# Kernel optimization log

Hardware: AMD Instinct MI355X
Metric: run time of the kernel (lower is better)

## Reference

```python
import jax, jax.numpy as jnp
import numpy as np

NUM_GROUPS = 64  # matches fill_max of ids; all groups present w.h.p. so unique-inverse == ids


def setup_inputs() -> dict:
    key = jax.random.key(0)
    ks = jax.random.split(key, 8)
    B, N, D = 8, 8192, 512
    s = 1.0 / np.sqrt(D)
    return {
        "x": jax.random.normal(ks[0], (B, N, D), dtype=jnp.float32),
        "ids": jax.random.randint(ks[1], (N,), 0, NUM_GROUPS),
        "w1": jax.random.normal(ks[2], (D, D), dtype=jnp.float32) * s,
        "b1": jax.random.normal(ks[3], (D,), dtype=jnp.float32) * s,
        "w2": jax.random.normal(ks[4], (D, D), dtype=jnp.float32) * s,
        "b2": jax.random.normal(ks[5], (D,), dtype=jnp.float32) * s,
        "w3": jax.random.normal(ks[6], (D, D), dtype=jnp.float32) * s,
        "b3": jax.random.normal(ks[7], (D,), dtype=jnp.float32) * s,
    }


def reference(x, ids, w1, b1, w2, b2, w3, b3):
    # x: [B, N, D]; ids: [N] group labels in [0, NUM_GROUPS)
    G = NUM_GROUPS
    a = jnp.einsum('bnd,ed->bne', x, w1) + b1          # linear1 logits
    v = jnp.einsum('bnd,ed->bne', x, w2) + b2          # linear2 values
    # move segment axis to front: [N, B, D]
    aT = jnp.transpose(a, (1, 0, 2))
    vT = jnp.transpose(v, (1, 0, 2))
    # per-group stable softmax along the segment axis
    mx = jax.lax.stop_gradient(jax.ops.segment_max(aT, ids, num_segments=G))  # [G,B,D]
    ex = jnp.exp(aT - mx[ids])
    denom = jax.ops.segment_sum(ex, ids, num_segments=G)                      # [G,B,D]
    wts = ex / denom[ids]                                                     # [N,B,D]
    # weighted scatter-sum of values -> [G, B, D] -> [B, G, D]
    y = jnp.transpose(jax.ops.segment_sum(vT * wts, ids, num_segments=G), (1, 0, 2))
    out = jnp.einsum('bgd,ed->bge', y, w3) + b3        # linear3
    # expand: gather group outputs back to per-element rows -> [B, N, D]
    return out[:, ids]
```

## Files before the change

### kernel.cpp

```cpp
#include <hip/hip_runtime.h>
#include <hip/hip_bf16.h>
#include <math.h>

#define B_ 8
#define N_ 8192
#define D_ 512
#define G_ 64
#define M_ (B_ * N_)

typedef short bf16x8 __attribute__((ext_vector_type(8)));
typedef float f32x4 __attribute__((ext_vector_type(4)));

__device__ __forceinline__ unsigned short f2bf(float f) {
    __hip_bfloat16 h = __float2bfloat16(f);
    return *reinterpret_cast<unsigned short*>(&h);
}
__device__ __forceinline__ void gload_lds16(const void* g, void* l) {
    __builtin_amdgcn_global_load_lds((const __attribute__((address_space(1))) void*)g,
                                     (__attribute__((address_space(3))) void*)l,
                                     16, 0, 0);
}

__global__ __launch_bounds__(256) void bl_all(const int* __restrict__ ids,
                                              int* __restrict__ counts,
                                              int* __restrict__ baseO,
                                              int* __restrict__ fgO,
                                              int* __restrict__ perm) {
    __shared__ int sid[N_];
    __shared__ unsigned short hist[256][G_];
    __shared__ int sb[G_ + 1];
    __shared__ int cnts[G_];
    const int g = blockIdx.x;
    const int t = threadIdx.x;
    for (int i = t; i < N_; i += 256) sid[i] = ids[i];
#pragma unroll
    for (int gg = 0; gg < G_; ++gg) hist[t][gg] = 0;
    __syncthreads();
    const int nb = t * 32;
    for (int k = 0; k < 32; ++k) hist[t][sid[nb + k]]++;
    __syncthreads();
    if (t < G_) {
        int run = 0;
        for (int i = 0; i < 256; ++i) {
            int v = hist[i][t];
            hist[i][t] = (unsigned short)run;
            run += v;
        }
        cnts[t] = run;
    }
    __syncthreads();
    if (t == 0) {
        int a = 0;
        for (int gg = 0; gg < G_; ++gg) { sb[gg] = a; a += cnts[gg]; }
        sb[G_] = a;
    }
    __syncthreads();
    if (g == 0 && t < G_) {
        counts[t] = cnts[t];
        baseO[t] = sb[t];
        const int row = t * 128;
        int gg = 0;
        while (gg + 1 < G_ && sb[gg + 1] <= row) ++gg;
        fgO[t] = gg;
    }
    int pos = sb[g] + hist[t][g];
    for (int k = 0; k < 32; ++k)
        if (sid[nb + k] == g) perm[pos++] = nb + k;
}

__global__ __launch_bounds__(256) void cast_all(const float* __restrict__ x,
                                                const int* __restrict__ perm,
                                                const float* __restrict__ w1,
                                                const float* __restrict__ b1,
                                                const float* __restrict__ w2,
                                                const float* __restrict__ b2,
                                                unsigned short* __restrict__ xb,
                                                unsigned short* __restrict__ wB,
                                                float* __restrict__ biasB) {
    const int bid = blockIdx.x;
    if (bid < 512) {
        int t = bid * 256 + threadIdx.x;
        int idx = t * 4;
        int row = idx >> 9;
        int col = idx & 511;
        const float* src = (row < 512) ? (w1 + (size_t)row * 512 + col)
                                       : (w2 + (size_t)(row - 512) * 512 + col);
        float4 f = *(const float4*)src;
        ushort4 u;
        u.x = f2bf(f.x); u.y = f2bf(f.y); u.z = f2bf(f.z); u.w = f2bf(f.w);
        *(ushort4*)(wB + idx) = u;
        if (t < 1024) biasB[t] = (t < 512) ? b1[t] : b2[t - 512];
    } else {
        const int total = M_ * 128;
        for (int idx = (bid - 512) * 256 + threadIdx.x; idx < total;
             idx += 2048 * 256) {
            const int row = idx >> 7;
            const int q = (idx & 127) * 4;
            const int b = row >> 13;
            const int i = row & 8191;
            const float* src = x + (((size_t)(b << 13) + perm[i]) << 9) + q;
            float4 f = *(const float4*)src;
            ushort4 u;
            u.x = f2bf(f.x); u.y = f2bf(f.y); u.z = f2bf(f.z); u.w = f2bf(f.w);
            *(ushort4*)(xb + ((size_t)row << 9) + q) = u;
        }
    }
}

__global__ __launch_bounds__(512, 2) void gemm_fused(const unsigned short* __restrict__ xb,
                                                     const unsigned short* __restrict__ wB,
                                                     const float* __restrict__ biasB,
                                                     const int* __restrict__ base,
                                                     const int* __restrict__ fg,
                                                     float* __restrict__ pt) {
    extern __shared__ unsigned short smem[];
    unsigned short* lsA = smem;
    unsigned short* lsB = smem + 32768;

    const int o  = blockIdx.x;
    const int mt = (o & 7) + ((o >> 5) << 3);
    const int nt = (o >> 3) & 3;
    const int b  = mt >> 5;
    const int tlb = (mt & 31) * 2;
    const int c0 = nt * 128;

    const int tid = threadIdx.x;
    const int l = tid & 63;
    const int w = tid >> 6;
    const int wm = w >> 2;
    const int wn = w & 3;
    const int lr = l >> 3;
    const int lslot = l & 7;
    const int fr = l & 15;
    const int kq = l >> 4;
    const int scol = 8 * (lslot ^ lr);

    f32x4 acc[8][4];
#pragma unroll
    for (int i = 0; i < 8; ++i)
#pragma unroll
        for (int j = 0; j < 4; ++j) acc[i][j] = (f32x4){0.f, 0.f, 0.f, 0.f};

    const size_t abase = (((size_t)b << 13) + (size_t)(mt & 31) * 256) << 9;

    auto stageT = [&](int buf, int kt) {
#pragma unroll
        for (int q = 0; q < 4; ++q) {
            const int c = w * 4 + q;
            const int row = c * 8 + lr;
            gload_lds16(xb + abase + ((size_t)row << 9) + kt + scol,
                        lsA + buf * 16384 + c * 512);
        }
#pragma unroll
        for (int q = 0; q < 4; ++q) {
            const int c = w * 4 + q;
            const int srcrow = ((c >> 2) & 1) * 512 + c0 + (c >> 3) * 32
                             + (c & 3) * 8 + lr;
            gload_lds16(wB + ((size_t)srcrow << 9) + kt + scol,
                        lsB + buf * 16384 + c * 512);
        }
    };

    stageT(0, 0);
    __syncthreads();
    int cur = 0;
    for (int t8 = 0; t8 < 8; ++t8) {
        if (t8 < 7) stageT(cur ^ 1, (t8 + 1) * 64);
        const unsigned short* pA = lsA + cur * 16384;
        const unsigned short* pB = lsB + cur * 16384;
        const int ib0 = 8 * (kq ^ (fr & 7));
        const int ib1 = 8 * ((4 + kq) ^ (fr & 7));
        bf16x8 bq0[4], bq1[4];
#pragma unroll
        for (int j = 0; j < 4; ++j) {
            const int brow = (wn * 64 + j * 16 + fr) * 64;
            bq0[j] = *(const bf16x8*)&pB[brow + ib0];
            bq1[j] = *(const bf16x8*)&pB[brow + ib1];
        }
#pragma unroll
        for (int i = 0; i < 8; ++i) {
            const int arow = (wm * 128 + i * 16 + fr) * 64;
            bf16x8 a0 = *(const bf16x8*)&pA[arow + ib0];
            bf16x8 a1 = *(const bf16x8*)&pA[arow + ib1];
#pragma unroll
            for (int j = 0; j < 4; ++j)
                acc[i][j] = __builtin_amdgcn_mfma_f32_16x16x32_bf16(a0, bq0[j], acc[i][j], 0, 0, 0);
#pragma unroll
            for (int j = 0; j < 4; ++j)
                acc[i][j] = __builtin_amdgcn_mfma_f32_16x16x32_bf16(a1, bq1[j], acc[i][j], 0, 0, 0);
        }
        __syncthreads();
        cur ^= 1;
    }

    const int tl = tlb + wm;
    const int fg0 = fg[tl];
    const int bnd0 = (fg0 + 1 < G_) ? base[fg0 + 1] : (1 << 30);
    const int bnd1 = (fg0 + 2 < G_) ? base[fg0 + 2] : (1 << 30);
    const int bnd2 = (fg0 + 3 < G_) ? base[fg0 + 3] : (1 << 30);
    float b1c[2], b2c[2];
#pragma unroll
    for (int j = 0; j < 2; ++j) {
        const int col = c0 + wn * 32 + j * 16 + fr;
        b1c[j] = biasB[col];
        b2c[j] = biasB[512 + col];
    }
    float dp[4][2] = {}, yp[4][2] = {};
    const int rbase = tl * 128 + kq * 4;
#pragma unroll
    for (int i = 0; i < 8; ++i)
#pragma unroll
        for (int rr = 0; rr < 4; ++rr) {
            const int row = rbase + i * 16 + rr;
            const int s = (row >= bnd0) + (row >= bnd1) + (row >= bnd2);
#pragma unroll
            for (int j = 0; j < 2; ++j) {
                const float e = __expf(acc[i][j][rr] + b1c[j]);
                const float ey = e * (acc[i][j + 2][rr] + b2c[j]);
#pragma unroll
                for (int s2 = 0; s2 < 4; ++s2) {
                    dp[s2][j] += (s == s2) ? e : 0.f;
                    yp[s2][j] += (s == s2) ? ey : 0.f;
                }
            }
        }
#pragma unroll
    for (int s2 = 0; s2 < 4; ++s2)
#pragma unroll
        for (int j = 0; j < 2; ++j) {
            dp[s2][j] += __shfl_xor(dp[s2][j], 16);
            dp[s2][j] += __shfl_xor(dp[s2][j], 32);
            yp[s2][j] += __shfl_xor(yp[s2][j], 16);
            yp[s2][j] += __shfl_xor(yp[s2][j], 32);
        }
    if (kq == 0) {
#pragma unroll
        for (int s2 = 0; s2 < 4; ++s2)
#pragma unroll
            for (int j = 0; j < 2; ++j) {
                const int colp = c0 + wn * 32 + j * 16 + fr;
                float2 v = make_float2(dp[s2][j], yp[s2][j]);
                *(float2*)&pt[(((size_t)(b * 64 + tl) * 4 + s2) * 512 + colp) * 2] = v;
            }
    }
}

__global__ __launch_bounds__(256) void combineC(const float* __restrict__ pt,
                                                const int* __restrict__ base,
                                                const int* __restrict__ counts,
                                                const int* __restrict__ fg,
                                                float* __restrict__ y) {
    const int g = blockIdx.x, b = blockIdx.y;
    const int bs = base[g];
    int cnt = counts[g];
    if (cnt == 0) cnt = 1;
    const int t0 = bs >> 7, t1 = (bs + cnt - 1) >> 7;
    for (int c = threadIdx.x; c < 512; c += 256) {
        float d = 0.f, yy = 0.f;
        for (int t = t0; t <= t1; ++t) {
            const int s = g - fg[t];
            if (s >= 0 && s < 4) {
                const float* p = &pt[((((size_t)(b * 64 + t)) * 4 + s) * 512 + c) * 2];
                d += p[0];
                yy += p[1];
            }
        }
        y[((size_t)(b * G_ + g)) * 512 + c] = yy / d;
    }
}

__global__ __launch_bounds__(256) void gemm3(const float* __restrict__ y,
                                             const float* __restrict__ w3,
                                             const float* __restrict__ b3,
                                             float* __restrict__ out_small) {
    __shared__ float ys[16][68];
    __shared__ float wss[16][68];
    const int m0 = blockIdx.x * 64;
    const int n0 = blockIdx.y * 64;
    const int tid = threadIdx.x;
    const int tr = tid >> 4;
    const int tc = tid & 15;
    const int lrow = tid >> 2;
    const int lk4 = (tid & 3) * 4;

    float acc[4][4] = {};

    for (int k0 = 0; k0 < D_; k0 += 16) {
        float4 yv = *(const float4*)(y + (size_t)(m0 + lrow) * D_ + k0 + lk4);
        float4 wv = *(const float4*)(w3 + (size_t)(n0 + lrow) * D_ + k0 + lk4);
        __syncthreads();
        ys[lk4 + 0][lrow] = yv.x;  ys[lk4 + 1][lrow] = yv.y;
        ys[lk4 + 2][lrow] = yv.z;  ys[lk4 + 3][lrow] = yv.w;
        wss[lk4 + 0][lrow] = wv.x; wss[lk4 + 1][lrow] = wv.y;
        wss[lk4 + 2][lrow] = wv.z; wss[lk4 + 3][lrow] = wv.w;
        __syncthreads();
#pragma unroll
        for (int kk = 0; kk < 16; ++kk) {
            float4 y4 = *(const float4*)&ys[kk][tr * 4];
            float4 w4 = *(const float4*)&wss[kk][tc * 4];
            float ya[4] = {y4.x, y4.y, y4.z, y4.w};
            float wa[4] = {w4.x, w4.y, w4.z, w4.w};
#pragma unroll
            for (int i = 0; i < 4; ++i)
#pragma unroll
                for (int j = 0; j < 4; ++j)
                    acc[i][j] = fmaf(ya[i], wa[j], acc[i][j]);
        }
    }

    float bb[4];
#pragma unroll
    for (int j = 0; j < 4; ++j) bb[j] = b3[n0 + tc * 4 + j];
#pragma unroll
    for (int i = 0; i < 4; ++i) {
        size_t o = (size_t)(m0 + tr * 4 + i) * D_ + n0 + tc * 4;
        float4 r;
        r.x = acc[i][0] + bb[0]; r.y = acc[i][1] + bb[1];
        r.z = acc[i][2] + bb[2]; r.w = acc[i][3] + bb[3];
        *(float4*)(out_small + o) = r;
    }
}

__global__ __launch_bounds__(256) void gather_out(const int* __restrict__ ids,
                                                  const float* __restrict__ out_small,
                                                  float* __restrict__ out) {
    const int c = blockIdx.x * 256 + threadIdx.x;
    const int per_row = D_ / 4;
    const int b = c / (N_ * per_row);
    const int rem = c % (N_ * per_row);
    const int n = rem / per_row;
    const int q = rem % per_row;
    const int g = ids[n];
    float4 val = *(const float4*)(out_small + ((size_t)b * G_ + g) * D_ + q * 4);
    *(float4*)(out + (size_t)c * 4) = val;
}

extern "C" void kernel_launch(void* const* d_in, const int* in_sizes, int n_in,
                              void* d_out, int out_size, void* d_ws, size_t ws_size,
                              hipStream_t stream) {
    (void)in_sizes; (void)n_in; (void)out_size; (void)ws_size;
    const float* x   = (const float*)d_in[0];
    const int*   ids = (const int*)d_in[1];
    const float* w1  = (const float*)d_in[2];
    const float* b1  = (const float*)d_in[3];
    const float* w2  = (const float*)d_in[4];
    const float* b2  = (const float*)d_in[5];
    const float* w3  = (const float*)d_in[6];
    const float* b3  = (const float*)d_in[7];
    float* out = (float*)d_out;

    float* ws_f = (float*)d_ws;
    unsigned short* xb = (unsigned short*)ws_f;
    float* after_xb  = ws_f + 16777216;
    unsigned short* wB = (unsigned short*)after_xb;
    float* biasB     = after_xb + 262144;
    float* pt        = biasB + 1024;
    float* y         = pt + 2097152;
    float* out_small = y + 262144;
    int*   perm      = (int*)(out_small + 262144);
    int*   base      = perm + N_;
    int*   counts    = base + G_;
    int*   fg        = counts + G_;

    hipFuncSetAttribute((const void*)gemm_fused,
                        hipFuncAttributeMaxDynamicSharedMemorySize, 131072);

    hipLaunchKernelGGL(bl_all, dim3(G_), dim3(256), 0, stream, ids, counts, base, fg, perm);
    hipLaunchKernelGGL(cast_all, dim3(2560), dim3(256), 0, stream,
                       x, perm, w1, b1, w2, b2, xb, wB, biasB);
    hipLaunchKernelGGL(gemm_fused, dim3(1024), dim3(512), 131072, stream,
                       xb, wB, biasB, base, fg, pt);
    hipLaunchKernelGGL(combineC, dim3(G_, B_), dim3(256), 0, stream, pt, base, counts, fg, y);
    hipLaunchKernelGGL(gemm3, dim3(8, 8), dim3(256), 0, stream, y, w3, b3, out_small);
    hipLaunchKernelGGL(gather_out, dim3(32768), dim3(256), 0, stream, ids, out_small, out);
}
```

Before: 193.3 us.

## Triple-buffer GEMM LDS pipeline with narrower N tiles and explicit vmcnt waits

The fused GEMM+softmax-reduction kernel moves from double to triple buffering. Each iteration issues loads two tiles ahead and waits with explicit s_waitcnt vmcnt counts plus raw barriers. The per-block N tile is halved (64 columns each of logits and values) and the grid doubled, which cuts accumulator registers. LDS use grows to 144KB and occupancy drops to one block per CU, trading occupancy for deeper prefetch and more blocks, each of which re-reads the A tile.

```diff
diff --git a/kernel.cpp b/kernel.cpp
--- a/kernel.cpp
+++ b/kernel.cpp
@@ -20,6 +20,7 @@
                                      (__attribute__((address_space(3))) void*)l,
                                      16, 0, 0);
 }
+#define SBAR() do { __builtin_amdgcn_s_barrier(); __builtin_amdgcn_sched_barrier(0); } while (0)
 
 __global__ __launch_bounds__(256) void bl_all(const int* __restrict__ ids,
                                               int* __restrict__ counts,
@@ -107,7 +108,7 @@
     }
 }
 
-__global__ __launch_bounds__(512, 2) void gemm_fused(const unsigned short* __restrict__ xb,
+__global__ __launch_bounds__(512, 1) void gemm_fused(const unsigned short* __restrict__ xb,
                                                      const unsigned short* __restrict__ wB,
                                                      const float* __restrict__ biasB,
                                                      const int* __restrict__ base,
@@ -115,14 +116,14 @@
                                                      float* __restrict__ pt) {
     extern __shared__ unsigned short smem[];
     unsigned short* lsA = smem;
-    unsigned short* lsB = smem + 32768;
+    unsigned short* lsB = smem + 3 * 16384;
 
     const int o  = blockIdx.x;
-    const int mt = (o & 7) + ((o >> 5) << 3);
-    const int nt = (o >> 3) & 3;
+    const int mt = (o & 7) + ((o >> 6) << 3);
+    const int nt = (o >> 3) & 7;
     const int b  = mt >> 5;
     const int tlb = (mt & 31) * 2;
-    const int c0 = nt * 128;
+    const int c0 = nt * 64;
 
     const int tid = threadIdx.x;
     const int l = tid & 63;
@@ -135,11 +136,12 @@
     const int kq = l >> 4;
     const int scol = 8 * (lslot ^ lr);
 
-    f32x4 acc[8][4];
-#pragma unroll
-    for (int i = 0; i < 8; ++i)
-#pragma unroll
-        for (int j = 0; j < 4; ++j) acc[i][j] = (f32x4){0.f, 0.f, 0.f, 0.f};
+    f32x4 acc[8][2];
+#pragma unroll
+    for (int i = 0; i < 8; ++i) {
+        acc[i][0] = (f32x4){0.f, 0.f, 0.f, 0.f};
+        acc[i][1] = (f32x4){0.f, 0.f, 0.f, 0.f};
+    }
 
     const size_t abase = (((size_t)b << 13) + (size_t)(mt & 31) * 256) << 9;
 
@@ -152,45 +154,41 @@
                         lsA + buf * 16384 + c * 512);
         }
 #pragma unroll
-        for (int q = 0; q < 4; ++q) {
-            const int c = w * 4 + q;
-            const int srcrow = ((c >> 2) & 1) * 512 + c0 + (c >> 3) * 32
-                             + (c & 3) * 8 + lr;
+        for (int q = 0; q < 2; ++q) {
+            const int c = w * 2 + q;
+            const int br = c * 8 + lr;
+            const int srcrow = (c >> 3) * 512 + c0 + (br & 63);
             gload_lds16(wB + ((size_t)srcrow << 9) + kt + scol,
-                        lsB + buf * 16384 + c * 512);
+                        lsB + buf * 8192 + c * 512);
         }
     };
 
     stageT(0, 0);
-    __syncthreads();
-    int cur = 0;
+    stageT(1, 64);
+
+#pragma unroll
     for (int t8 = 0; t8 < 8; ++t8) {
-        if (t8 < 7) stageT(cur ^ 1, (t8 + 1) * 64);
-        const unsigned short* pA = lsA + cur * 16384;
-        const unsigned short* pB = lsB + cur * 16384;
-        const int ib0 = 8 * (kq ^ (fr & 7));
-        const int ib1 = 8 * ((4 + kq) ^ (fr & 7));
-        bf16x8 bq0[4], bq1[4];
-#pragma unroll
-        for (int j = 0; j < 4; ++j) {
-            const int brow = (wn * 64 + j * 16 + fr) * 64;
-            bq0[j] = *(const bf16x8*)&pB[brow + ib0];
-            bq1[j] = *(const bf16x8*)&pB[brow + ib1];
-        }
-#pragma unroll
-        for (int i = 0; i < 8; ++i) {
-            const int arow = (wm * 128 + i * 16 + fr) * 64;
-            bf16x8 a0 = *(const bf16x8*)&pA[arow + ib0];
-            bf16x8 a1 = *(const bf16x8*)&pA[arow + ib1];
-#pragma unroll
-            for (int j = 0; j < 4; ++j)
-                acc[i][j] = __builtin_amdgcn_mfma_f32_16x16x32_bf16(a0, bq0[j], acc[i][j], 0, 0, 0);
-#pragma unroll
-            for (int j = 0; j < 4; ++j)
-                acc[i][j] = __builtin_amdgcn_mfma_f32_16x16x32_bf16(a1, bq1[j], acc[i][j], 0, 0, 0);
-        }
-        __syncthreads();
-        cur ^= 1;
+        SBAR();
+        if (t8 < 6) stageT((t8 + 2) % 3, (t8 + 2) * 64);
+        if (t8 < 6)      asm volatile("s_waitcnt vmcnt(12)" ::: "memory");
+        else if (t8 == 6) asm volatile("s_waitcnt vmcnt(6)" ::: "memory");
+        else              asm volatile("s_waitcnt vmcnt(0)" ::: "memory");
+        __builtin_amdgcn_sched_barrier(0);
+        SBAR();
+        const unsigned short* pA = lsA + (t8 % 3) * 16384;
+        const unsigned short* pB = lsB + (t8 % 3) * 8192;
+#pragma unroll
+        for (int ks = 0; ks < 2; ++ks) {
+            const int ib = 8 * ((ks * 4 + kq) ^ (fr & 7));
+            bf16x8 ba = *(const bf16x8*)&pB[(wn * 16 + fr) * 64 + ib];
+            bf16x8 bv = *(const bf16x8*)&pB[(64 + wn * 16 + fr) * 64 + ib];
+#pragma unroll
+            for (int i = 0; i < 8; ++i) {
+                bf16x8 a = *(const bf16x8*)&pA[(wm * 128 + i * 16 + fr) * 64 + ib];
+                acc[i][0] = __builtin_amdgcn_mfma_f32_16x16x32_bf16(a, ba, acc[i][0], 0, 0, 0);
+                acc[i][1] = __builtin_amdgcn_mfma_f32_16x16x32_bf16(a, bv, acc[i][1], 0, 0, 0);
+            }
+        }
     }
 
     const int tl = tlb + wm;
@@ -198,14 +196,10 @@
     const int bnd0 = (fg0 + 1 < G_) ? base[fg0 + 1] : (1 << 30);
     const int bnd1 = (fg0 + 2 < G_) ? base[fg0 + 2] : (1 << 30);
     const int bnd2 = (fg0 + 3 < G_) ? base[fg0 + 3] : (1 << 30);
-    float b1c[2], b2c[2];
-#pragma unroll
-    for (int j = 0; j < 2; ++j) {
-        const int col = c0 + wn * 32 + j * 16 + fr;
-        b1c[j] = biasB[col];
-        b2c[j] = biasB[512 + col];
-    }
-    float dp[4][2] = {}, yp[4][2] = {};
+    const int colp = c0 + wn * 16 + fr;
+    const float b1c = biasB[colp];
+    const float b2c = biasB[512 + colp];
+    float dp[4] = {}, yp[4] = {};
     const int rbase = tl * 128 + kq * 4;
 #pragma unroll
     for (int i = 0; i < 8; ++i)
@@ -213,35 +207,27 @@
         for (int rr = 0; rr < 4; ++rr) {
             const int row = rbase + i * 16 + rr;
             const int s = (row >= bnd0) + (row >= bnd1) + (row >= bnd2);
-#pragma unroll
-            for (int j = 0; j < 2; ++j) {
-                const float e = __expf(acc[i][j][rr] + b1c[j]);
-                const float ey = e * (acc[i][j + 2][rr] + b2c[j]);
-#pragma unroll
-                for (int s2 = 0; s2 < 4; ++s2) {
-                    dp[s2][j] += (s == s2) ? e : 0.f;
-                    yp[s2][j] += (s == s2) ? ey : 0.f;
-                }
+            const float e = __expf(acc[i][0][rr] + b1c);
+            const float ey = e * (acc[i][1][rr] + b2c);
+#pragma unroll
+            for (int s2 = 0; s2 < 4; ++s2) {
+                dp[s2] += (s == s2) ? e : 0.f;
+                yp[s2] += (s == s2) ? ey : 0.f;
             }
         }
 #pragma unroll
-    for (int s2 = 0; s2 < 4; ++s2)
-#pragma unroll
-        for (int j = 0; j < 2; ++j) {
-            dp[s2][j] += __shfl_xor(dp[s2][j], 16);
-            dp[s2][j] += __shfl_xor(dp[s2][j], 32);
-            yp[s2][j] += __shfl_xor(yp[s2][j], 16);
-            yp[s2][j] += __shfl_xor(yp[s2][j], 32);
-        }
+    for (int s2 = 0; s2 < 4; ++s2) {
+        dp[s2] += __shfl_xor(dp[s2], 16);
+        dp[s2] += __shfl_xor(dp[s2], 32);
+        yp[s2] += __shfl_xor(yp[s2], 16);
+        yp[s2] += __shfl_xor(yp[s2], 32);
+    }
     if (kq == 0) {
 #pragma unroll
-        for (int s2 = 0; s2 < 4; ++s2)
-#pragma unroll
-            for (int j = 0; j < 2; ++j) {
-                const int colp = c0 + wn * 32 + j * 16 + fr;
-                float2 v = make_float2(dp[s2][j], yp[s2][j]);
-                *(float2*)&pt[(((size_t)(b * 64 + tl) * 4 + s2) * 512 + colp) * 2] = v;
-            }
+        for (int s2 = 0; s2 < 4; ++s2) {
+            float2 v = make_float2(dp[s2], yp[s2]);
+            *(float2*)&pt[(((size_t)(b * 64 + tl) * 4 + s2) * 512 + colp) * 2] = v;
+        }
     }
 }
 
@@ -363,12 +349,12 @@
     int*   fg        = counts + G_;
 
     hipFuncSetAttribute((const void*)gemm_fused,
-                        hipFuncAttributeMaxDynamicSharedMemorySize, 131072);
+                        hipFuncAttributeMaxDynamicSharedMemorySize, 147456);
 
     hipLaunchKernelGGL(bl_all, dim3(G_), dim3(256), 0, stream, ids, counts, base, fg, perm);
     hipLaunchKernelGGL(cast_all, dim3(2560), dim3(256), 0, stream,
                        x, perm, w1, b1, w2, b2, xb, wB, biasB);
-    hipLaunchKernelGGL(gemm_fused, dim3(1024), dim3(512), 131072, stream,
+    hipLaunchKernelGGL(gemm_fused, dim3(2048), dim3(512), 147456, stream,
                        xb, wB, biasB, base, fg, pt);
     hipLaunchKernelGGL(combineC, dim3(G_, B_), dim3(256), 0, stream, pt, base, counts, fg, y);
     hipLaunchKernelGGL(gemm3, dim3(8, 8), dim3(256), 0, stream, y, w3, b3, out_small);
```

Result: slower. 207.2 us (+7.2%).

## Load weight fragments directly into registers, halving LDS use in fused GEMM

Applied to the files above, without the earlier changes.

The weight (B) tile is no longer staged through shared memory. Each lane now loads its MFMA B fragments straight from global memory into double-buffered registers, prefetching the next k-step. This halves dynamic LDS from 128KB to 64KB, which may allow more blocks per CU and removes the LDS reads for B. The cost is uncoalesced-ish global loads, duplicated B loads across the waves that share a column slice, and extra register pressure under launch_bounds(512,2).

```diff
diff --git a/kernel.cpp b/kernel.cpp
--- a/kernel.cpp
+++ b/kernel.cpp
@@ -115,7 +115,6 @@
                                                      float* __restrict__ pt) {
     extern __shared__ unsigned short smem[];
     unsigned short* lsA = smem;
-    unsigned short* lsB = smem + 32768;
 
     const int o  = blockIdx.x;
     const int mt = (o & 7) + ((o >> 5) << 3);
@@ -151,32 +150,37 @@
             gload_lds16(xb + abase + ((size_t)row << 9) + kt + scol,
                         lsA + buf * 16384 + c * 512);
         }
-#pragma unroll
-        for (int q = 0; q < 4; ++q) {
-            const int c = w * 4 + q;
-            const int srcrow = ((c >> 2) & 1) * 512 + c0 + (c >> 3) * 32
-                             + (c & 3) * 8 + lr;
-            gload_lds16(wB + ((size_t)srcrow << 9) + kt + scol,
-                        lsB + buf * 16384 + c * 512);
-        }
     };
 
+    const unsigned short* bptr[4];
+#pragma unroll
+    for (int j = 0; j < 4; ++j) {
+        const int srcrow = (j >= 2 ? 512 : 0) + c0 + wn * 32 + (j & 1) * 16 + fr;
+        bptr[j] = wB + ((size_t)srcrow << 9) + kq * 8;
+    }
+    auto loadB = [&](int kt, bf16x8 (&dst)[8]) {
+#pragma unroll
+        for (int j = 0; j < 4; ++j) {
+            dst[j * 2 + 0] = *(const bf16x8*)(bptr[j] + kt);
+            dst[j * 2 + 1] = *(const bf16x8*)(bptr[j] + kt + 32);
+        }
+    };
+
+    bf16x8 breg[2][8];
+    loadB(0, breg[0]);
     stageT(0, 0);
     __syncthreads();
-    int cur = 0;
+
+#pragma unroll
     for (int t8 = 0; t8 < 8; ++t8) {
-        if (t8 < 7) stageT(cur ^ 1, (t8 + 1) * 64);
-        const unsigned short* pA = lsA + cur * 16384;
-        const unsigned short* pB = lsB + cur * 16384;
+        const int cb = t8 & 1;
+        if (t8 < 7) {
+            stageT(cb ^ 1, (t8 + 1) * 64);
+            loadB((t8 + 1) * 64, breg[cb ^ 1]);
+        }
+        const unsigned short* pA = lsA + cb * 16384;
         const int ib0 = 8 * (kq ^ (fr & 7));
         const int ib1 = 8 * ((4 + kq) ^ (fr & 7));
-        bf16x8 bq0[4], bq1[4];
-#pragma unroll
-        for (int j = 0; j < 4; ++j) {
-            const int brow = (wn * 64 + j * 16 + fr) * 64;
-            bq0[j] = *(const bf16x8*)&pB[brow + ib0];
-            bq1[j] = *(const bf16x8*)&pB[brow + ib1];
-        }
 #pragma unroll
         for (int i = 0; i < 8; ++i) {
             const int arow = (wm * 128 + i * 16 + fr) * 64;
@@ -184,13 +188,12 @@
             bf16x8 a1 = *(const bf16x8*)&pA[arow + ib1];
 #pragma unroll
             for (int j = 0; j < 4; ++j)
-                acc[i][j] = __builtin_amdgcn_mfma_f32_16x16x32_bf16(a0, bq0[j], acc[i][j], 0, 0, 0);
+                acc[i][j] = __builtin_amdgcn_mfma_f32_16x16x32_bf16(a0, breg[cb][j * 2], acc[i][j], 0, 0, 0);
 #pragma unroll
             for (int j = 0; j < 4; ++j)
-                acc[i][j] = __builtin_amdgcn_mfma_f32_16x16x32_bf16(a1, bq1[j], acc[i][j], 0, 0, 0);
+                acc[i][j] = __builtin_amdgcn_mfma_f32_16x16x32_bf16(a1, breg[cb][j * 2 + 1], acc[i][j], 0, 0, 0);
         }
         __syncthreads();
-        cur ^= 1;
     }
 
     const int tl = tlb + wm;
@@ -363,12 +366,12 @@
     int*   fg        = counts + G_;
 
     hipFuncSetAttribute((const void*)gemm_fused,
-                        hipFuncAttributeMaxDynamicSharedMemorySize, 131072);
+                        hipFuncAttributeMaxDynamicSharedMemorySize, 65536);
 
     hipLaunchKernelGGL(bl_all, dim3(G_), dim3(256), 0, stream, ids, counts, base, fg, perm);
     hipLaunchKernelGGL(cast_all, dim3(2560), dim3(256), 0, stream,
                        x, perm, w1, b1, w2, b2, xb, wB, biasB);
-    hipLaunchKernelGGL(gemm_fused, dim3(1024), dim3(512), 131072, stream,
+    hipLaunchKernelGGL(gemm_fused, dim3(1024), dim3(512), 65536, stream,
                        xb, wB, biasB, base, fg, pt);
     hipLaunchKernelGGL(combineC, dim3(G_, B_), dim3(256), 0, stream, pt, base, counts, fg, y);
     hipLaunchKernelGGL(gemm3, dim3(8, 8), dim3(256), 0, stream, y, w3, b3, out_small);
```

New measurement: 231.4 us. 19.7% more time.
